# Optimization experiments

Hardware: AMD Instinct MI355X
Metric: run time of the kernel (lower is better)

The kernel has to match this reference:

```python
import jax, jax.numpy as jnp
import numpy as np

NUM_HEADS = 16


def setup_inputs() -> dict:
    key = jax.random.key(0)
    ks = jax.random.split(key, 9)
    B, N, E = 2, 2048, 1024
    s = 1.0 / np.sqrt(E).astype(np.float32)
    inp = {"x": jax.random.normal(ks[0], (B, N, E), jnp.float32)}
    names = ["q", "k", "v", "o"]
    for i, n in enumerate(names):
        inp[f"W{n}"] = jax.random.normal(ks[1 + 2 * i], (E, E), jnp.float32) * s
        inp[f"b{n}"] = jax.random.normal(ks[2 + 2 * i], (E,), jnp.float32) * 0.01
    return inp


def _feature(x):
    # act_fun = '1+elu'
    return jax.nn.elu(x) + 1.0


def reference(x, Wq, bq, Wk, bk, Wv, bv, Wo, bo):
    B, N, E = x.shape
    H = NUM_HEADS
    d = E // H

    def proj(t, W, b):  # torch nn.Linear: t @ W^T + b
        return t @ W.T + b

    def split_heads(t):  # (B,N,E) -> (B,H,N,d)
        return t.reshape(B, N, H, d).transpose(0, 2, 1, 3)

    q = _feature(split_heads(proj(x, Wq, bq)))
    k = _feature(split_heads(proj(x, Wk, bk)))
    v = split_heads(proj(x, Wv, bv))

    # causal linear attention: o_t = q_t @ cumsum_{s<=t} (k_s v_s^T)
    kv = jnp.cumsum(k[..., :, None] * v[..., None, :], axis=2)  # (B,H,N,d,d)
    o = jnp.einsum('bhnd,bhnde->bhne', q, kv)                   # (B,H,N,d)

    o = o.transpose(0, 2, 1, 3).reshape(B, N, E)
    return o @ Wo.T + bo
```

## Files before the change

kernel.cpp:

```cpp
#include <hip/hip_runtime.h>
#include <hip/hip_bf16.h>
#include <cmath>

typedef unsigned short u16;
typedef __bf16 bf16x8 __attribute__((ext_vector_type(8)));
typedef float  f32x4  __attribute__((ext_vector_type(4)));
typedef float  f4     __attribute__((ext_vector_type(4)));
typedef u16    us4    __attribute__((ext_vector_type(4)));

#define DEVFN __device__ __forceinline__

static constexpr int Bq = 2, Nq = 2048, Eq = 1024;
static constexpr int Mq = Bq * Nq;
static constexpr int CHK = 64;
static constexpr int NC  = Nq / CHK;
static constexpr int BH  = Bq * 16;

DEVFN u16 f2b(float f) {
    union { float f; unsigned int u; } x; x.f = f;
    unsigned int r = x.u + 0x7fffu + ((x.u >> 16) & 1u);
    return (u16)(r >> 16);
}
DEVFN float b2f(u16 v) {
    union { unsigned int u; float f; } x; x.u = ((unsigned int)v) << 16; return x.f;
}

DEVFN void gl_lds16(const u16* g, u16* l) {
    __builtin_amdgcn_global_load_lds(
        (const __attribute__((address_space(1))) unsigned int*)(g),
        (__attribute__((address_space(3))) unsigned int*)(l),
        16, 0, 0);
}

__global__ __launch_bounds__(256)
void cvt_all_kernel(const float* __restrict__ x,
                    const float* __restrict__ w0, const float* __restrict__ w1,
                    const float* __restrict__ w2, const float* __restrict__ w3,
                    u16* __restrict__ Xb, u16* __restrict__ Wb)
{
    const int blk = blockIdx.x;
    const float* s; u16* d; int i;
    if (blk < 4096) {
        i = blk * 256 + threadIdx.x;  s = x;  d = Xb;
    } else {
        const int wsel = (blk - 4096) >> 10;
        i = ((blk - 4096) & 1023) * 256 + threadIdx.x;
        s = (wsel == 0) ? w0 : (wsel == 1) ? w1 : (wsel == 2) ? w2 : w3;
        d = Wb + (size_t)wsel * (Eq * Eq);
    }
    f4 v = *reinterpret_cast<const f4*>(&s[(size_t)i * 4]);
    us4 p; p[0] = f2b(v[0]); p[1] = f2b(v[1]); p[2] = f2b(v[2]); p[3] = f2b(v[3]);
    *reinterpret_cast<us4*>(&d[(size_t)i * 4]) = p;
}

template<int MODE>
__global__ __launch_bounds__(128, 2)
void gemm_ring(const u16* __restrict__ X, const u16* __restrict__ W,
               const float* __restrict__ b0, const float* __restrict__ b1,
               const float* __restrict__ b2,
               u16* __restrict__ Qb, u16* __restrict__ Kb, u16* __restrict__ KbT,
               u16* __restrict__ VbT, float* __restrict__ outF)
{
    constexpr int BM   = (MODE == 0) ? 128 : 64;
    constexpr int MI   = BM / 32;
    constexpr int AR   = BM / 32;
    constexpr int BUFU = (BM + 128) * 32;
    constexpr int NT   = 32;
    __shared__ u16 lds[3 * BUFU];

    const int tid = threadIdx.x, wid = tid >> 6, lane = tid & 63;
    const int bid = blockIdx.x;
    const int fid = (MODE == 0) ? ((bid & 7) * 96 + (bid >> 3))
                                : ((bid & 7) * 64 + (bid >> 3));
    const int bx  = (MODE == 0) ? (fid % 24) : (fid & 7);
    const int by  = (MODE == 0) ? (fid / 24) : (fid >> 3);
    const int m0  = by * BM, n0 = bx * 128;
    const int wr  = wid * (BM / 2);
    const int fr  = lane & 15, fq = lane >> 4;

    const int row0 = tid >> 2;
    const int ssw  = ((tid & 3) ^ ((row0 >> 1) & 3)) * 8;
    const u16* gA = X + (size_t)(m0 + row0) * 1024 + ssw;
    const u16* gB = W + (size_t)(n0 + row0) * 1024 + ssw;
    const int dstA = wid * 512;
    const int dstB = BM * 32 + wid * 512;

    const int fsw = (fq ^ ((fr >> 1) & 3)) << 3;
    int aoff[MI], boff[8];
#pragma unroll
    for (int mi = 0; mi < MI; ++mi) aoff[mi] = (wr + mi * 16 + fr) * 32 + fsw;
#pragma unroll
    for (int ni = 0; ni < 8; ++ni)  boff[ni] = BM * 32 + (ni * 16 + fr) * 32 + fsw;

#define STAGE(kt, bsel) do {                                                   \
        const int _k = (kt) * 32;                                              \
        u16* _b = lds + (bsel) * BUFU;                                         \
        _Pragma("unroll")                                                      \
        for (int it = 0; it < AR; ++it)                                        \
            gl_lds16(gA + _k + (size_t)it * 32 * 1024, _b + dstA + it * 1024); \
        _Pragma("unroll")                                                      \
        for (int it = 0; it < 4; ++it)                                         \
            gl_lds16(gB + _k + (size_t)it * 32 * 1024, _b + dstB + it * 1024); \
    } while (0)

#define VM_WAIT_STEADY() do {                                                  \
        if (MODE == 0) asm volatile("s_waitcnt vmcnt(8)" ::: "memory");        \
        else           asm volatile("s_waitcnt vmcnt(6)" ::: "memory");        \
    } while (0)

    STAGE(0, 0);
    STAGE(1, 1);
    VM_WAIT_STEADY();
    __builtin_amdgcn_sched_barrier(0);
    __builtin_amdgcn_s_barrier();

    f32x4 acc[MI][8] = {};
    int cb = 0, sb = 2;

    for (int t = 0; t < NT; ++t) {
        if (t + 2 < NT) STAGE(t + 2, sb);
        const u16* buf = lds + cb * BUFU;
        bf16x8 af[MI], bfv[8];
#pragma unroll
        for (int mi = 0; mi < MI; ++mi)
            af[mi] = *reinterpret_cast<const bf16x8*>(&buf[aoff[mi]]);
#pragma unroll
        for (int ni = 0; ni < 8; ++ni)
            bfv[ni] = *reinterpret_cast<const bf16x8*>(&buf[boff[ni]]);
        __builtin_amdgcn_s_setprio(1);
#pragma unroll
        for (int mi = 0; mi < MI; ++mi)
#pragma unroll
            for (int ni = 0; ni < 8; ++ni)
                acc[mi][ni] = __builtin_amdgcn_mfma_f32_16x16x32_bf16(
                    af[mi], bfv[ni], acc[mi][ni], 0, 0, 0);
        __builtin_amdgcn_s_setprio(0);
        if (t < NT - 2)       VM_WAIT_STEADY();
        else if (t == NT - 2) asm volatile("s_waitcnt vmcnt(0)" ::: "memory");
        __builtin_amdgcn_sched_barrier(0);
        __builtin_amdgcn_s_barrier();
        cb = (cb == 2) ? 0 : cb + 1;
        sb = (sb == 2) ? 0 : sb + 1;
    }
#undef STAGE
#undef VM_WAIT_STEADY

    if (MODE == 0) {
        const int seg = n0 >> 10;
        const float* bp = (seg == 0) ? b0 : (seg == 1) ? b1 : b2;
#pragma unroll
        for (int mi = 0; mi < MI; ++mi)
#pragma unroll
            for (int ni = 0; ni < 8; ++ni) {
                const int nl    = (n0 & 1023) + ni * 16 + fr;
                const int mbase = m0 + wr + mi * 16 + fq * 4;
                const float bn  = bp[nl];
                float vr[4];
#pragma unroll
                for (int r = 0; r < 4; ++r) {
                    float v = acc[mi][ni][r] + bn;
                    if (seg < 2) v = (v > 0.f) ? (v + 1.f) : __expf(v);
                    vr[r] = v;
                }
                if (seg == 0) {
#pragma unroll
                    for (int r = 0; r < 4; ++r)
                        Qb[(size_t)(mbase + r) * 1024 + nl] = f2b(vr[r]);
                } else {
                    us4 pk;
#pragma unroll
                    for (int r = 0; r < 4; ++r) pk[r] = f2b(vr[r]);
                    const int bb = mbase >> 11, nt = mbase & 2047;
                    const int hh = nl >> 6,     dd = nl & 63;
                    u16* T = (seg == 1) ? KbT : VbT;
                    *reinterpret_cast<us4*>(
                        &T[((size_t)(bb * 16 + hh) * 64 + dd) * 2048 + nt]) = pk;
                    if (seg == 1) {
#pragma unroll
                        for (int r = 0; r < 4; ++r)
                            Kb[(size_t)(mbase + r) * 1024 + nl] = f2b(vr[r]);
                    }
                }
            }
    } else {
#pragma unroll
        for (int mi = 0; mi < MI; ++mi)
#pragma unroll
            for (int ni = 0; ni < 8; ++ni) {
                const int n     = n0 + ni * 16 + fr;
                const int mbase = m0 + wr + mi * 16 + fq * 4;
                const float bn  = b0[n];
#pragma unroll
                for (int r = 0; r < 4; ++r)
                    outF[(size_t)(mbase + r) * 1024 + n] = acc[mi][ni][r] + bn;
            }
    }
}

__global__ __launch_bounds__(64)
void chunk_kv_kernel(const u16* __restrict__ KbT, const u16* __restrict__ VbT,
                     u16* __restrict__ KVT)
{
    const int blk = blockIdx.x;
    const int bh = blk >> 5, c = blk & 31;
    const int lane = threadIdx.x;
    const int fr = lane & 15, fq = lane >> 4, fk = fq * 8;
    const u16* kt = KbT + (size_t)bh * 64 * 2048;
    const u16* vt = VbT + (size_t)bh * 64 * 2048;

    bf16x8 a[4][2], b[4][2];
#pragma unroll
    for (int mi = 0; mi < 4; ++mi)
#pragma unroll
        for (int kh = 0; kh < 2; ++kh)
            a[mi][kh] = *reinterpret_cast<const bf16x8*>(
                &vt[(size_t)(mi * 16 + fr) * 2048 + c * 64 + kh * 32 + fk]);
#pragma unroll
    for (int ni = 0; ni < 4; ++ni)
#pragma unroll
        for (int kh = 0; kh < 2; ++kh)
            b[ni][kh] = *reinterpret_cast<const bf16x8*>(
                &kt[(size_t)(ni * 16 + fr) * 2048 + c * 64 + kh * 32 + fk]);

    f32x4 acc[4][4] = {};
    __builtin_amdgcn_s_setprio(1);
#pragma unroll
    for (int mi = 0; mi < 4; ++mi)
#pragma unroll
        for (int ni = 0; ni < 4; ++ni)
#pragma unroll
            for (int kh = 0; kh < 2; ++kh)
                acc[mi][ni] = __builtin_amdgcn_mfma_f32_16x16x32_bf16(
                    a[mi][kh], b[ni][kh], acc[mi][ni], 0, 0, 0);
    __builtin_amdgcn_s_setprio(0);

    u16* out = KVT + (size_t)blk * 4096;
#pragma unroll
    for (int mi = 0; mi < 4; ++mi)
#pragma unroll
        for (int ni = 0; ni < 4; ++ni)
#pragma unroll
            for (int r = 0; r < 4; ++r)
                out[(mi * 16 + fq * 4 + r) * 64 + ni * 16 + fr] = f2b(acc[mi][ni][r]);
}

__global__ __launch_bounds__(256)
void scan_kernel(const u16* __restrict__ KVT, u16* __restrict__ STb)
{
    const int bh = blockIdx.x >> 4, sl = blockIdx.x & 15;
    const int el = sl * 256 + threadIdx.x;
    const u16* src = KVT + (size_t)bh * NC * 4096 + el;
    u16*      dst  = STb + (size_t)bh * NC * 4096 + el;
    float run = 0.f;
#pragma unroll 4
    for (int c = 0; c < NC; ++c) {
        dst[(size_t)c * 4096] = f2b(run);
        run += b2f(src[(size_t)c * 4096]);
    }
}

__global__ __launch_bounds__(64)
void attn_kernel(const u16* __restrict__ Qb, const u16* __restrict__ Kb,
                 const u16* __restrict__ VbT, const u16* __restrict__ STb,
                 u16* __restrict__ Ob)
{
    __shared__ u16 P[64 * 72];
    const int blk = blockIdx.x;
    const int bh = blk >> 5, c = blk & 31;
    const int b = bh >> 4, h = bh & 15;
    const int lane = threadIdx.x;
    const int fr = lane & 15, fq = lane >> 4, fk = fq * 8;
    const int tok0 = b * 2048 + c * 64;

    bf16x8 qa[4][2];
#pragma unroll
    for (int mi = 0; mi < 4; ++mi)
#pragma unroll
        for (int kh = 0; kh < 2; ++kh)
            qa[mi][kh] = *reinterpret_cast<const bf16x8*>(
                &Qb[(size_t)(tok0 + mi * 16 + fr) * 1024 + h * 64 + kh * 32 + fk]);

    {
        bf16x8 kb[4][2];
#pragma unroll
        for (int si = 0; si < 4; ++si)
#pragma unroll
            for (int kh = 0; kh < 2; ++kh)
                kb[si][kh] = *reinterpret_cast<const bf16x8*>(
                    &Kb[(size_t)(tok0 + si * 16 + fr) * 1024 + h * 64 + kh * 32 + fk]);
        f32x4 p[4][4] = {};
        __builtin_amdgcn_s_setprio(1);
#pragma unroll
        for (int mi = 0; mi < 4; ++mi)
#pragma unroll
            for (int si = 0; si < 4; ++si)
#pragma unroll
                for (int kh = 0; kh < 2; ++kh)
                    p[mi][si] = __builtin_amdgcn_mfma_f32_16x16x32_bf16(
                        qa[mi][kh], kb[si][kh], p[mi][si], 0, 0, 0);
        __builtin_amdgcn_s_setprio(0);
#pragma unroll
        for (int mi = 0; mi < 4; ++mi)
#pragma unroll
            for (int si = 0; si < 4; ++si)
#pragma unroll
                for (int r = 0; r < 4; ++r) {
                    int t = mi * 16 + fq * 4 + r;
                    int s = si * 16 + fr;
                    float v = (s <= t) ? p[mi][si][r] : 0.0f;
                    P[t * 72 + s] = f2b(v);
                }
    }
    __syncthreads();

    f32x4 acc[4][4] = {};
    {
        const u16* st = STb + (size_t)blk * 4096;
        bf16x8 sb[4][2];
#pragma unroll
        for (int ni = 0; ni < 4; ++ni)
#pragma unroll
            for (int kh = 0; kh < 2; ++kh)
                sb[ni][kh] = *reinterpret_cast<const bf16x8*>(
                    &st[(ni * 16 + fr) * 64 + kh * 32 + fk]);
        __builtin_amdgcn_s_setprio(1);
#pragma unroll
        for (int mi = 0; mi < 4; ++mi)
#pragma unroll
            for (int ni = 0; ni < 4; ++ni)
#pragma unroll
                for (int kh = 0; kh < 2; ++kh)
                    acc[mi][ni] = __builtin_amdgcn_mfma_f32_16x16x32_bf16(
                        qa[mi][kh], sb[ni][kh], acc[mi][ni], 0, 0, 0);
        __builtin_amdgcn_s_setprio(0);
    }
    {
        const u16* vt = VbT + (size_t)bh * 64 * 2048;
#pragma unroll
        for (int sh = 0; sh < 2; ++sh) {
            bf16x8 pa[4], vb[4];
#pragma unroll
            for (int mi = 0; mi < 4; ++mi)
                pa[mi] = *reinterpret_cast<const bf16x8*>(
                    &P[(mi * 16 + fr) * 72 + sh * 32 + fk]);
#pragma unroll
            for (int ni = 0; ni < 4; ++ni)
                vb[ni] = *reinterpret_cast<const bf16x8*>(
                    &vt[(size_t)(ni * 16 + fr) * 2048 + c * 64 + sh * 32 + fk]);
            __builtin_amdgcn_s_setprio(1);
#pragma unroll
            for (int mi = 0; mi < 4; ++mi)
#pragma unroll
                for (int ni = 0; ni < 4; ++ni)
                    acc[mi][ni] = __builtin_amdgcn_mfma_f32_16x16x32_bf16(
                        pa[mi], vb[ni], acc[mi][ni], 0, 0, 0);
            __builtin_amdgcn_s_setprio(0);
        }
    }
#pragma unroll
    for (int mi = 0; mi < 4; ++mi)
#pragma unroll
        for (int ni = 0; ni < 4; ++ni)
#pragma unroll
            for (int r = 0; r < 4; ++r) {
                int t = tok0 + mi * 16 + fq * 4 + r;
                int n = h * 64 + ni * 16 + fr;
                Ob[(size_t)t * 1024 + n] = f2b(acc[mi][ni][r]);
            }
}

extern "C" void kernel_launch(void* const* d_in, const int* in_sizes, int n_in,
                              void* d_out, int out_size, void* d_ws, size_t ws_size,
                              hipStream_t stream)
{
    (void)in_sizes; (void)n_in; (void)out_size; (void)ws_size;
    const float* x  = (const float*)d_in[0];
    const float* Wq = (const float*)d_in[1];
    const float* bq = (const float*)d_in[2];
    const float* Wk = (const float*)d_in[3];
    const float* bk = (const float*)d_in[4];
    const float* Wv = (const float*)d_in[5];
    const float* bv = (const float*)d_in[6];
    const float* Wo = (const float*)d_in[7];
    const float* bo = (const float*)d_in[8];
    float* out = (float*)d_out;

    char* ws = (char*)d_ws;
    constexpr size_t SZ_ME = (size_t)Mq * Eq * 2;
    u16*   Qb  = (u16*)  (ws + 0 * SZ_ME);
    u16*   Kb  = (u16*)  (ws + 1 * SZ_ME);
    u16*   KbT = (u16*)  (ws + 2 * SZ_ME);
    u16*   VbT = (u16*)  (ws + 3 * SZ_ME);
    u16*   Ob  = (u16*)  (ws + 4 * SZ_ME);
    u16*   KVT = (u16*)  (ws + 5 * SZ_ME);
    u16*   STb = (u16*)  (ws + 6 * SZ_ME);
    u16*   Xb  = (u16*)  (ws + 7 * SZ_ME);
    u16*   Wb0 = (u16*)  (ws + 8 * SZ_ME);
    u16* Wqkvb = Wb0;
    u16* Wob   = Wb0 + (size_t)3 * Eq * Eq;

    cvt_all_kernel<<<dim3(8192), dim3(256), 0, stream>>>(x, Wq, Wk, Wv, Wo, Xb, Wb0);

    gemm_ring<0><<<dim3(768), dim3(128), 0, stream>>>(
        Xb, Wqkvb, bq, bk, bv, Qb, Kb, KbT, VbT, nullptr);

    chunk_kv_kernel<<<dim3(BH * NC), dim3(64), 0, stream>>>(KbT, VbT, KVT);
    scan_kernel<<<dim3(BH * 16), dim3(256), 0, stream>>>(KVT, STb);
    attn_kernel<<<dim3(BH * NC), dim3(64), 0, stream>>>(Qb, Kb, VbT, STb, Ob);

    gemm_ring<1><<<dim3(512), dim3(128), 0, stream>>>(
        Ob, Wob, bo, nullptr, nullptr, nullptr, nullptr, nullptr, nullptr, out);
}
```

Before: 94.66 us.

## Replace LDS-staged GEMM ring with direct global-to-register MFMA loads

Both projection GEMMs drop the three-stage LDS ring buffer fed by global_load_lds. Each of four waves now loads its own MFMA fragments straight from global memory into registers, double-buffered across k-steps, with an occasional block barrier to keep the waves loosely in step. This removes LDS traffic and the per-step barriers, but gives up the in-block sharing of A/B tiles, so global/L2 load volume rises and the per-lane 16-byte row-strided loads may coalesce poorly.

```diff
diff --git a/kernel.cpp b/kernel.cpp
--- a/kernel.cpp
+++ b/kernel.cpp
@@ -23,13 +23,6 @@
 }
 DEVFN float b2f(u16 v) {
     union { unsigned int u; float f; } x; x.u = ((unsigned int)v) << 16; return x.f;
-}
-
-DEVFN void gl_lds16(const u16* g, u16* l) {
-    __builtin_amdgcn_global_load_lds(
-        (const __attribute__((address_space(1))) unsigned int*)(g),
-        (__attribute__((address_space(3))) unsigned int*)(l),
-        16, 0, 0);
 }
 
 __global__ __launch_bounds__(256)
@@ -54,96 +47,64 @@
 }
 
 template<int MODE>
-__global__ __launch_bounds__(128, 2)
-void gemm_ring(const u16* __restrict__ X, const u16* __restrict__ W,
-               const float* __restrict__ b0, const float* __restrict__ b1,
-               const float* __restrict__ b2,
-               u16* __restrict__ Qb, u16* __restrict__ Kb, u16* __restrict__ KbT,
-               u16* __restrict__ VbT, float* __restrict__ outF)
-{
-    constexpr int BM   = (MODE == 0) ? 128 : 64;
-    constexpr int MI   = BM / 32;
-    constexpr int AR   = BM / 32;
-    constexpr int BUFU = (BM + 128) * 32;
-    constexpr int NT   = 32;
-    __shared__ u16 lds[3 * BUFU];
-
+__global__ __launch_bounds__(256)
+void gemm_direct(const u16* __restrict__ X, const u16* __restrict__ W,
+                 const float* __restrict__ b0, const float* __restrict__ b1,
+                 const float* __restrict__ b2,
+                 u16* __restrict__ Qb, u16* __restrict__ Kb, u16* __restrict__ KbT,
+                 u16* __restrict__ VbT, float* __restrict__ outF)
+{
+    constexpr int MI = (MODE == 0) ? 4 : 2;
     const int tid = threadIdx.x, wid = tid >> 6, lane = tid & 63;
+    const int fr = lane & 15, fq = lane >> 4;
     const int bid = blockIdx.x;
     const int fid = (MODE == 0) ? ((bid & 7) * 96 + (bid >> 3))
                                 : ((bid & 7) * 64 + (bid >> 3));
     const int bx  = (MODE == 0) ? (fid % 24) : (fid & 7);
     const int by  = (MODE == 0) ? (fid / 24) : (fid >> 3);
-    const int m0  = by * BM, n0 = bx * 128;
-    const int wr  = wid * (BM / 2);
-    const int fr  = lane & 15, fq = lane >> 4;
-
-    const int row0 = tid >> 2;
-    const int ssw  = ((tid & 3) ^ ((row0 >> 1) & 3)) * 8;
-    const u16* gA = X + (size_t)(m0 + row0) * 1024 + ssw;
-    const u16* gB = W + (size_t)(n0 + row0) * 1024 + ssw;
-    const int dstA = wid * 512;
-    const int dstB = BM * 32 + wid * 512;
-
-    const int fsw = (fq ^ ((fr >> 1) & 3)) << 3;
-    int aoff[MI], boff[8];
-#pragma unroll
-    for (int mi = 0; mi < MI; ++mi) aoff[mi] = (wr + mi * 16 + fr) * 32 + fsw;
-#pragma unroll
-    for (int ni = 0; ni < 8; ++ni)  boff[ni] = BM * 32 + (ni * 16 + fr) * 32 + fsw;
-
-#define STAGE(kt, bsel) do {                                                   \
-        const int _k = (kt) * 32;                                              \
-        u16* _b = lds + (bsel) * BUFU;                                         \
-        _Pragma("unroll")                                                      \
-        for (int it = 0; it < AR; ++it)                                        \
-            gl_lds16(gA + _k + (size_t)it * 32 * 1024, _b + dstA + it * 1024); \
-        _Pragma("unroll")                                                      \
-        for (int it = 0; it < 4; ++it)                                         \
-            gl_lds16(gB + _k + (size_t)it * 32 * 1024, _b + dstB + it * 1024); \
+    const int m0  = (MODE == 0) ? (by * 128 + (wid >> 1) * 64)
+                                : (by * 64  + (wid >> 1) * 32);
+    const int n0  = bx * 128 + (wid & 1) * 64;
+
+    const u16* pa[MI];
+    const u16* pb[4];
+#pragma unroll
+    for (int mi = 0; mi < MI; ++mi)
+        pa[mi] = X + (size_t)(m0 + mi * 16 + fr) * 1024 + fq * 8;
+#pragma unroll
+    for (int ni = 0; ni < 4; ++ni)
+        pb[ni] = W + (size_t)(n0 + ni * 16 + fr) * 1024 + fq * 8;
+
+#define LD(as, bs, t) do {                                                   \
+        _Pragma("unroll")                                                    \
+        for (int mi = 0; mi < MI; ++mi)                                      \
+            as[mi] = *reinterpret_cast<const bf16x8*>(pa[mi] + (t) * 32);    \
+        _Pragma("unroll")                                                    \
+        for (int ni = 0; ni < 4; ++ni)                                       \
+            bs[ni] = *reinterpret_cast<const bf16x8*>(pb[ni] + (t) * 32);    \
     } while (0)
-
-#define VM_WAIT_STEADY() do {                                                  \
-        if (MODE == 0) asm volatile("s_waitcnt vmcnt(8)" ::: "memory");        \
-        else           asm volatile("s_waitcnt vmcnt(6)" ::: "memory");        \
+#define FM(as, bs) do {                                                      \
+        _Pragma("unroll")                                                    \
+        for (int mi = 0; mi < MI; ++mi)                                      \
+            _Pragma("unroll")                                                \
+            for (int ni = 0; ni < 4; ++ni)                                   \
+                acc[mi][ni] = __builtin_amdgcn_mfma_f32_16x16x32_bf16(       \
+                    as[mi], bs[ni], acc[mi][ni], 0, 0, 0);                   \
     } while (0)
 
-    STAGE(0, 0);
-    STAGE(1, 1);
-    VM_WAIT_STEADY();
-    __builtin_amdgcn_sched_barrier(0);
-    __builtin_amdgcn_s_barrier();
-
-    f32x4 acc[MI][8] = {};
-    int cb = 0, sb = 2;
-
-    for (int t = 0; t < NT; ++t) {
-        if (t + 2 < NT) STAGE(t + 2, sb);
-        const u16* buf = lds + cb * BUFU;
-        bf16x8 af[MI], bfv[8];
-#pragma unroll
-        for (int mi = 0; mi < MI; ++mi)
-            af[mi] = *reinterpret_cast<const bf16x8*>(&buf[aoff[mi]]);
-#pragma unroll
-        for (int ni = 0; ni < 8; ++ni)
-            bfv[ni] = *reinterpret_cast<const bf16x8*>(&buf[boff[ni]]);
-        __builtin_amdgcn_s_setprio(1);
-#pragma unroll
-        for (int mi = 0; mi < MI; ++mi)
-#pragma unroll
-            for (int ni = 0; ni < 8; ++ni)
-                acc[mi][ni] = __builtin_amdgcn_mfma_f32_16x16x32_bf16(
-                    af[mi], bfv[ni], acc[mi][ni], 0, 0, 0);
-        __builtin_amdgcn_s_setprio(0);
-        if (t < NT - 2)       VM_WAIT_STEADY();
-        else if (t == NT - 2) asm volatile("s_waitcnt vmcnt(0)" ::: "memory");
-        __builtin_amdgcn_sched_barrier(0);
-        __builtin_amdgcn_s_barrier();
-        cb = (cb == 2) ? 0 : cb + 1;
-        sb = (sb == 2) ? 0 : sb + 1;
-    }
-#undef STAGE
-#undef VM_WAIT_STEADY
+    f32x4 acc[MI][4] = {};
+    bf16x8 aX[MI], bX[4], aY[MI], bY[4];
+    LD(aX, bX, 0);
+#pragma unroll 4
+    for (int t = 0; t < 32; t += 2) {
+        LD(aY, bY, t + 1);
+        FM(aX, bX);
+        if (t + 2 < 32) LD(aX, bX, t + 2);
+        FM(aY, bY);
+        if ((t & 7) == 6) __builtin_amdgcn_s_barrier();
+    }
+#undef LD
+#undef FM
 
     if (MODE == 0) {
         const int seg = n0 >> 10;
@@ -151,9 +112,9 @@
 #pragma unroll
         for (int mi = 0; mi < MI; ++mi)
 #pragma unroll
-            for (int ni = 0; ni < 8; ++ni) {
+            for (int ni = 0; ni < 4; ++ni) {
                 const int nl    = (n0 & 1023) + ni * 16 + fr;
-                const int mbase = m0 + wr + mi * 16 + fq * 4;
+                const int mbase = m0 + mi * 16 + fq * 4;
                 const float bn  = bp[nl];
                 float vr[4];
 #pragma unroll
@@ -186,9 +147,9 @@
 #pragma unroll
         for (int mi = 0; mi < MI; ++mi)
 #pragma unroll
-            for (int ni = 0; ni < 8; ++ni) {
+            for (int ni = 0; ni < 4; ++ni) {
                 const int n     = n0 + ni * 16 + fr;
-                const int mbase = m0 + wr + mi * 16 + fq * 4;
+                const int mbase = m0 + mi * 16 + fq * 4;
                 const float bn  = b0[n];
 #pragma unroll
                 for (int r = 0; r < 4; ++r)
@@ -401,13 +362,13 @@
 
     cvt_all_kernel<<<dim3(8192), dim3(256), 0, stream>>>(x, Wq, Wk, Wv, Wo, Xb, Wb0);
 
-    gemm_ring<0><<<dim3(768), dim3(128), 0, stream>>>(
+    gemm_direct<0><<<dim3(768), dim3(256), 0, stream>>>(
         Xb, Wqkvb, bq, bk, bv, Qb, Kb, KbT, VbT, nullptr);
 
     chunk_kv_kernel<<<dim3(BH * NC), dim3(64), 0, stream>>>(KbT, VbT, KVT);
     scan_kernel<<<dim3(BH * 16), dim3(256), 0, stream>>>(KVT, STb);
     attn_kernel<<<dim3(BH * NC), dim3(64), 0, stream>>>(Qb, Kb, VbT, STb, Ob);
 
-    gemm_ring<1><<<dim3(512), dim3(128), 0, stream>>>(
+    gemm_direct<1><<<dim3(512), dim3(256), 0, stream>>>(
         Ob, Wob, bo, nullptr, nullptr, nullptr, nullptr, nullptr, nullptr, out);
 }
```

After: 186.8 us. +97.3%, slower.

## Use 256x256 8-wave tiles for QKV GEMM and 4-wave O-projection kernel

Applied to the files above, without the earlier changes.

Replaces the templated 2-wave GEMM with a dedicated QKV kernel using 512-thread blocks computing 256x256 tiles (2x4 wave grid). Loads of A and B halves are interleaved between two MFMA phases inside each k-step. The output projection gets its own 256-thread kernel that splits a 64x128 tile across 4 waves. The larger QKV tile raises data reuse per LDS load and cuts global traffic. In exchange it adds extra barriers, uses only 192 blocks for 256 CUs, and raises register pressure from 32 accumulators per wave.

```diff
diff --git a/kernel.cpp b/kernel.cpp
--- a/kernel.cpp
+++ b/kernel.cpp
@@ -53,148 +53,218 @@
     *reinterpret_cast<us4*>(&d[(size_t)i * 4]) = p;
 }
 
-template<int MODE>
-__global__ __launch_bounds__(128, 2)
-void gemm_ring(const u16* __restrict__ X, const u16* __restrict__ W,
-               const float* __restrict__ b0, const float* __restrict__ b1,
-               const float* __restrict__ b2,
-               u16* __restrict__ Qb, u16* __restrict__ Kb, u16* __restrict__ KbT,
-               u16* __restrict__ VbT, float* __restrict__ outF)
-{
-    constexpr int BM   = (MODE == 0) ? 128 : 64;
-    constexpr int MI   = BM / 32;
-    constexpr int AR   = BM / 32;
-    constexpr int BUFU = (BM + 128) * 32;
-    constexpr int NT   = 32;
-    __shared__ u16 lds[3 * BUFU];
-
+__global__ __launch_bounds__(512, 2)
+void qkv8_kernel(const u16* __restrict__ X, const u16* __restrict__ W,
+                 const float* __restrict__ b0, const float* __restrict__ b1,
+                 const float* __restrict__ b2,
+                 u16* __restrict__ Qb, u16* __restrict__ Kb, u16* __restrict__ KbT,
+                 u16* __restrict__ VbT)
+{
+    __shared__ u16 lds[3 * 16384];
     const int tid = threadIdx.x, wid = tid >> 6, lane = tid & 63;
+    const int wm = wid >> 2, wn = wid & 3;
+    const int fr = lane & 15, fq = lane >> 4;
+
     const int bid = blockIdx.x;
-    const int fid = (MODE == 0) ? ((bid & 7) * 96 + (bid >> 3))
-                                : ((bid & 7) * 64 + (bid >> 3));
-    const int bx  = (MODE == 0) ? (fid % 24) : (fid & 7);
-    const int by  = (MODE == 0) ? (fid / 24) : (fid >> 3);
-    const int m0  = by * BM, n0 = bx * 128;
-    const int wr  = wid * (BM / 2);
-    const int fr  = lane & 15, fq = lane >> 4;
-
-    const int row0 = tid >> 2;
-    const int ssw  = ((tid & 3) ^ ((row0 >> 1) & 3)) * 8;
-    const u16* gA = X + (size_t)(m0 + row0) * 1024 + ssw;
-    const u16* gB = W + (size_t)(n0 + row0) * 1024 + ssw;
-    const int dstA = wid * 512;
-    const int dstB = BM * 32 + wid * 512;
+    const int fid = (bid & 7) * 24 + (bid >> 3);
+    const int bx = fid % 12, by = fid / 12;
+    const int m0 = by * 256, n0 = bx * 256;
+
+    const int ra = tid >> 2;
+    const int sc = ((tid & 3) ^ ((tid >> 3) & 3)) * 8;
+    const u16* gA = X + (size_t)(m0 + ra) * 1024 + sc;
+    const u16* gB = W + (size_t)(n0 + ra) * 1024 + sc;
+    const int dw = wid * 512;
 
     const int fsw = (fq ^ ((fr >> 1) & 3)) << 3;
-    int aoff[MI], boff[8];
-#pragma unroll
-    for (int mi = 0; mi < MI; ++mi) aoff[mi] = (wr + mi * 16 + fr) * 32 + fsw;
-#pragma unroll
-    for (int ni = 0; ni < 8; ++ni)  boff[ni] = BM * 32 + (ni * 16 + fr) * 32 + fsw;
-
-#define STAGE(kt, bsel) do {                                                   \
-        const int _k = (kt) * 32;                                              \
-        u16* _b = lds + (bsel) * BUFU;                                         \
-        _Pragma("unroll")                                                      \
-        for (int it = 0; it < AR; ++it)                                        \
-            gl_lds16(gA + _k + (size_t)it * 32 * 1024, _b + dstA + it * 1024); \
-        _Pragma("unroll")                                                      \
-        for (int it = 0; it < 4; ++it)                                         \
-            gl_lds16(gB + _k + (size_t)it * 32 * 1024, _b + dstB + it * 1024); \
-    } while (0)
-
-#define VM_WAIT_STEADY() do {                                                  \
-        if (MODE == 0) asm volatile("s_waitcnt vmcnt(8)" ::: "memory");        \
-        else           asm volatile("s_waitcnt vmcnt(6)" ::: "memory");        \
-    } while (0)
-
-    STAGE(0, 0);
-    STAGE(1, 1);
-    VM_WAIT_STEADY();
+    int aoff[2][4], boff[4];
+#pragma unroll
+    for (int h = 0; h < 2; ++h)
+#pragma unroll
+        for (int j = 0; j < 4; ++j)
+            aoff[h][j] = (wm * 128 + h * 64 + j * 16 + fr) * 32 + fsw;
+#pragma unroll
+    for (int j = 0; j < 4; ++j)
+        boff[j] = 8192 + (wn * 64 + j * 16 + fr) * 32 + fsw;
+
+#define STA(kt, bs) do { u16* _b = lds + (bs) * 16384 + dw;                      \
+        gl_lds16(gA + (kt) * 32,              _b);                               \
+        gl_lds16(gA + (kt) * 32 + 128 * 1024, _b + 4096); } while (0)
+#define STB(kt, bs) do { u16* _b = lds + (bs) * 16384 + 8192 + dw;               \
+        gl_lds16(gB + (kt) * 32,              _b);                               \
+        gl_lds16(gB + (kt) * 32 + 128 * 1024, _b + 4096); } while (0)
+
+    STA(0, 0); STB(0, 0);
+    STA(1, 1); STB(1, 1);
+    asm volatile("s_waitcnt vmcnt(4)" ::: "memory");
     __builtin_amdgcn_sched_barrier(0);
     __builtin_amdgcn_s_barrier();
 
-    f32x4 acc[MI][8] = {};
+    f32x4 acc[8][4] = {};
     int cb = 0, sb = 2;
 
-    for (int t = 0; t < NT; ++t) {
-        if (t + 2 < NT) STAGE(t + 2, sb);
-        const u16* buf = lds + cb * BUFU;
-        bf16x8 af[MI], bfv[8];
-#pragma unroll
-        for (int mi = 0; mi < MI; ++mi)
-            af[mi] = *reinterpret_cast<const bf16x8*>(&buf[aoff[mi]]);
-#pragma unroll
-        for (int ni = 0; ni < 8; ++ni)
-            bfv[ni] = *reinterpret_cast<const bf16x8*>(&buf[boff[ni]]);
+    for (int t = 0; t < 32; ++t) {
+        const u16* buf = lds + cb * 16384;
+        bf16x8 a[4], b[4];
+#pragma unroll
+        for (int j = 0; j < 4; ++j)
+            a[j] = *reinterpret_cast<const bf16x8*>(&buf[aoff[0][j]]);
+#pragma unroll
+        for (int j = 0; j < 4; ++j)
+            b[j] = *reinterpret_cast<const bf16x8*>(&buf[boff[j]]);
+        if (t + 2 < 32) STA(t + 2, sb);
+        __builtin_amdgcn_s_barrier();
         __builtin_amdgcn_s_setprio(1);
 #pragma unroll
-        for (int mi = 0; mi < MI; ++mi)
-#pragma unroll
-            for (int ni = 0; ni < 8; ++ni)
-                acc[mi][ni] = __builtin_amdgcn_mfma_f32_16x16x32_bf16(
-                    af[mi], bfv[ni], acc[mi][ni], 0, 0, 0);
+        for (int j = 0; j < 4; ++j)
+#pragma unroll
+            for (int n = 0; n < 4; ++n)
+                acc[j][n] = __builtin_amdgcn_mfma_f32_16x16x32_bf16(
+                    a[j], b[n], acc[j][n], 0, 0, 0);
         __builtin_amdgcn_s_setprio(0);
-        if (t < NT - 2)       VM_WAIT_STEADY();
-        else if (t == NT - 2) asm volatile("s_waitcnt vmcnt(0)" ::: "memory");
+        __builtin_amdgcn_s_barrier();
+#pragma unroll
+        for (int j = 0; j < 4; ++j)
+            a[j] = *reinterpret_cast<const bf16x8*>(&buf[aoff[1][j]]);
+        if (t + 2 < 32) STB(t + 2, sb);
+        __builtin_amdgcn_s_barrier();
+        __builtin_amdgcn_s_setprio(1);
+#pragma unroll
+        for (int j = 0; j < 4; ++j)
+#pragma unroll
+            for (int n = 0; n < 4; ++n)
+                acc[4 + j][n] = __builtin_amdgcn_mfma_f32_16x16x32_bf16(
+                    a[j], b[n], acc[4 + j][n], 0, 0, 0);
+        __builtin_amdgcn_s_setprio(0);
+        if (t < 30)       asm volatile("s_waitcnt vmcnt(4)" ::: "memory");
+        else if (t == 30) asm volatile("s_waitcnt vmcnt(0)" ::: "memory");
         __builtin_amdgcn_sched_barrier(0);
         __builtin_amdgcn_s_barrier();
         cb = (cb == 2) ? 0 : cb + 1;
         sb = (sb == 2) ? 0 : sb + 1;
     }
-#undef STAGE
-#undef VM_WAIT_STEADY
-
-    if (MODE == 0) {
-        const int seg = n0 >> 10;
-        const float* bp = (seg == 0) ? b0 : (seg == 1) ? b1 : b2;
-#pragma unroll
-        for (int mi = 0; mi < MI; ++mi)
-#pragma unroll
-            for (int ni = 0; ni < 8; ++ni) {
-                const int nl    = (n0 & 1023) + ni * 16 + fr;
-                const int mbase = m0 + wr + mi * 16 + fq * 4;
-                const float bn  = bp[nl];
-                float vr[4];
-#pragma unroll
-                for (int r = 0; r < 4; ++r) {
-                    float v = acc[mi][ni][r] + bn;
-                    if (seg < 2) v = (v > 0.f) ? (v + 1.f) : __expf(v);
-                    vr[r] = v;
-                }
-                if (seg == 0) {
+#undef STA
+#undef STB
+
+    const int nw  = n0 + wn * 64;
+    const int seg = nw >> 10;
+    const float* bp = (seg == 0) ? b0 : (seg == 1) ? b1 : b2;
+#pragma unroll
+    for (int mg = 0; mg < 8; ++mg)
+#pragma unroll
+        for (int ni = 0; ni < 4; ++ni) {
+            const int nl    = ((nw & 1023) + ni * 16 + fr);
+            const int mbase = m0 + wm * 128 + mg * 16 + fq * 4;
+            const float bn  = bp[nl];
+            float vr[4];
+#pragma unroll
+            for (int r = 0; r < 4; ++r) {
+                float v = acc[mg][ni][r] + bn;
+                if (seg < 2) v = (v > 0.f) ? (v + 1.f) : __expf(v);
+                vr[r] = v;
+            }
+            if (seg == 0) {
+#pragma unroll
+                for (int r = 0; r < 4; ++r)
+                    Qb[(size_t)(mbase + r) * 1024 + nl] = f2b(vr[r]);
+            } else {
+                us4 pk;
+#pragma unroll
+                for (int r = 0; r < 4; ++r) pk[r] = f2b(vr[r]);
+                const int bb = mbase >> 11, nt = mbase & 2047;
+                const int hh = nl >> 6,     dd = nl & 63;
+                u16* T = (seg == 1) ? KbT : VbT;
+                *reinterpret_cast<us4*>(
+                    &T[((size_t)(bb * 16 + hh) * 64 + dd) * 2048 + nt]) = pk;
+                if (seg == 1) {
 #pragma unroll
                     for (int r = 0; r < 4; ++r)
-                        Qb[(size_t)(mbase + r) * 1024 + nl] = f2b(vr[r]);
-                } else {
-                    us4 pk;
-#pragma unroll
-                    for (int r = 0; r < 4; ++r) pk[r] = f2b(vr[r]);
-                    const int bb = mbase >> 11, nt = mbase & 2047;
-                    const int hh = nl >> 6,     dd = nl & 63;
-                    u16* T = (seg == 1) ? KbT : VbT;
-                    *reinterpret_cast<us4*>(
-                        &T[((size_t)(bb * 16 + hh) * 64 + dd) * 2048 + nt]) = pk;
-                    if (seg == 1) {
-#pragma unroll
-                        for (int r = 0; r < 4; ++r)
-                            Kb[(size_t)(mbase + r) * 1024 + nl] = f2b(vr[r]);
-                    }
+                        Kb[(size_t)(mbase + r) * 1024 + nl] = f2b(vr[r]);
                 }
             }
-    } else {
-#pragma unroll
-        for (int mi = 0; mi < MI; ++mi)
-#pragma unroll
-            for (int ni = 0; ni < 8; ++ni) {
-                const int n     = n0 + ni * 16 + fr;
-                const int mbase = m0 + wr + mi * 16 + fq * 4;
-                const float bn  = b0[n];
-#pragma unroll
-                for (int r = 0; r < 4; ++r)
-                    outF[(size_t)(mbase + r) * 1024 + n] = acc[mi][ni][r] + bn;
-            }
-    }
+        }
+}
+
+__global__ __launch_bounds__(256)
+void oproj_kernel(const u16* __restrict__ X, const u16* __restrict__ W,
+                  const float* __restrict__ b0, float* __restrict__ outF)
+{
+    constexpr int BUFU = (64 + 128) * 32;
+    __shared__ u16 lds[3 * BUFU];
+    const int tid = threadIdx.x, wid = tid >> 6, lane = tid & 63;
+    const int wr = (wid >> 1) * 32, wc = (wid & 1) * 64;
+    const int fr = lane & 15, fq = lane >> 4;
+
+    const int bid = blockIdx.x;
+    const int fid = (bid & 7) * 64 + (bid >> 3);
+    const int bx = fid & 7, by = fid >> 3;
+    const int m0 = by * 64, n0 = bx * 128;
+
+    const int ra = tid >> 2;
+    const int sc = ((tid & 3) ^ ((tid >> 3) & 3)) * 8;
+    const u16* gA = X + (size_t)(m0 + ra) * 1024 + sc;
+    const u16* gB = W + (size_t)(n0 + ra) * 1024 + sc;
+    const int dw = wid * 512;
+
+    const int fsw = (fq ^ ((fr >> 1) & 3)) << 3;
+    int aoff[2], boff[4];
+#pragma unroll
+    for (int mi = 0; mi < 2; ++mi) aoff[mi] = (wr + mi * 16 + fr) * 32 + fsw;
+#pragma unroll
+    for (int ni = 0; ni < 4; ++ni) boff[ni] = 2048 + (wc + ni * 16 + fr) * 32 + fsw;
+
+#define STAGE(kt, bs) do { u16* _b = lds + (bs) * BUFU;                          \
+        gl_lds16(gA + (kt) * 32,             _b + dw);                           \
+        gl_lds16(gB + (kt) * 32,             _b + 2048 + dw);                    \
+        gl_lds16(gB + (kt) * 32 + 64 * 1024, _b + 4096 + dw); } while (0)
+
+    STAGE(0, 0);
+    STAGE(1, 1);
+    asm volatile("s_waitcnt vmcnt(3)" ::: "memory");
+    __builtin_amdgcn_sched_barrier(0);
+    __builtin_amdgcn_s_barrier();
+
+    f32x4 acc[2][4] = {};
+    int cb = 0, sb = 2;
+
+    for (int t = 0; t < 32; ++t) {
+        if (t + 2 < 32) STAGE(t + 2, sb);
+        const u16* buf = lds + cb * BUFU;
+        bf16x8 af[2], bfv[4];
+#pragma unroll
+        for (int mi = 0; mi < 2; ++mi)
+            af[mi] = *reinterpret_cast<const bf16x8*>(&buf[aoff[mi]]);
+#pragma unroll
+        for (int ni = 0; ni < 4; ++ni)
+            bfv[ni] = *reinterpret_cast<const bf16x8*>(&buf[boff[ni]]);
+        __builtin_amdgcn_s_setprio(1);
+#pragma unroll
+        for (int mi = 0; mi < 2; ++mi)
+#pragma unroll
+            for (int ni = 0; ni < 4; ++ni)
+                acc[mi][ni] = __builtin_amdgcn_mfma_f32_16x16x32_bf16(
+                    af[mi], bfv[ni], acc[mi][ni], 0, 0, 0);
+        __builtin_amdgcn_s_setprio(0);
+        if (t < 30)       asm volatile("s_waitcnt vmcnt(3)" ::: "memory");
+        else if (t == 30) asm volatile("s_waitcnt vmcnt(0)" ::: "memory");
+        __builtin_amdgcn_sched_barrier(0);
+        __builtin_amdgcn_s_barrier();
+        cb = (cb == 2) ? 0 : cb + 1;
+        sb = (sb == 2) ? 0 : sb + 1;
+    }
+#undef STAGE
+
+#pragma unroll
+    for (int mi = 0; mi < 2; ++mi)
+#pragma unroll
+        for (int ni = 0; ni < 4; ++ni) {
+            const int n     = n0 + wc + ni * 16 + fr;
+            const int mbase = m0 + wr + mi * 16 + fq * 4;
+            const float bn  = b0[n];
+#pragma unroll
+            for (int r = 0; r < 4; ++r)
+                outF[(size_t)(mbase + r) * 1024 + n] = acc[mi][ni][r] + bn;
+        }
 }
 
 __global__ __launch_bounds__(64)
@@ -401,13 +471,12 @@
 
     cvt_all_kernel<<<dim3(8192), dim3(256), 0, stream>>>(x, Wq, Wk, Wv, Wo, Xb, Wb0);
 
-    gemm_ring<0><<<dim3(768), dim3(128), 0, stream>>>(
-        Xb, Wqkvb, bq, bk, bv, Qb, Kb, KbT, VbT, nullptr);
+    qkv8_kernel<<<dim3(192), dim3(512), 0, stream>>>(
+        Xb, Wqkvb, bq, bk, bv, Qb, Kb, KbT, VbT);
 
     chunk_kv_kernel<<<dim3(BH * NC), dim3(64), 0, stream>>>(KbT, VbT, KVT);
     scan_kernel<<<dim3(BH * 16), dim3(256), 0, stream>>>(KVT, STb);
     attn_kernel<<<dim3(BH * NC), dim3(64), 0, stream>>>(Qb, Kb, VbT, STb, Ob);
 
-    gemm_ring<1><<<dim3(512), dim3(128), 0, stream>>>(
-        Ob, Wob, bo, nullptr, nullptr, nullptr, nullptr, nullptr, nullptr, out);
-}
+    oproj_kernel<<<dim3(512), dim3(256), 0, stream>>>(Ob, Wob, bo, out);
+}
```

Measured after the change: 95.36 us. Within noise of the previous version (+0.7%).
